# Optimization experiments

Measured on AMD Instinct MI355X. Metric: run time of the kernel, lower is better.

Reference implementation:

```python
import jax, jax.numpy as jnp
import numpy as np

B, D, C = 8192, 2048, 1000
EPS32 = float(np.finfo(np.float32).eps)      # torch clamp_probs uses finfo.eps
LOG_2PI = float(np.log(2.0 * np.pi))
GAMMA = float(1.0 / np.exp(100.0))           # lerp at global_step=0 -> start_val = 1/exp(start_rho)


def setup_inputs() -> dict:
    key = jax.random.key(0)
    k = jax.random.split(key, 6)
    feature = jax.random.normal(k[0], (B, D), jnp.float32)
    target = jax.random.randint(k[1], (B,), 0, C)
    eps = jax.random.normal(k[2], (B, D), jnp.float32)
    # y_project: Linear(C, D) -> weight [D, C], bias [D]
    y_w = jax.random.normal(k[3], (D, C), jnp.float32) * 0.02
    y_b = jnp.zeros((D,), jnp.float32)
    # cls_project: Linear(D, C) -> weight [C, D], bias [C]
    # small weights + positive bias keep Categorical probs positive (torch would
    # clamp negatives to eps; we replicate the clamp but avoid degenerate NaNs)
    cls_w = jax.random.normal(k[4], (C, D), jnp.float32) * 0.001
    cls_b = jnp.ones((C,), jnp.float32) * 5.0
    return dict(feature=feature, y_w=y_w, y_b=y_b, cls_w=cls_w, cls_b=cls_b,
                eps=eps, target=target)


def reference(feature, y_w, y_b, cls_w, cls_b, eps, target):
    # z = m.sample() : identity-covariance MVN sample, detached (torch .sample())
    z = jax.lax.stop_gradient(feature + eps)                      # [B, D]

    # y_emb = y_project(one_hot(target)) == gather of weight columns + bias
    y_emb = jnp.take(y_w, target, axis=1).T + y_b                 # [B, D]

    # Categorical(probs=cls_project(z)): normalize, clamp, log
    probs_raw = z @ cls_w.T + cls_b                               # [B, C]
    p = probs_raw / jnp.sum(probs_raw, axis=-1, keepdims=True)
    logits = jnp.log(jnp.clip(p, EPS32, 1.0 - EPS32))             # [B, C]

    # identity-covariance MVN log_prob in closed form
    const = 0.5 * D * LOG_2PI
    h1 = 0.5 * jnp.sum((z - feature) ** 2, axis=-1) + const       # -m.log_prob(z)
    h2 = 0.5 * jnp.sum((z - y_emb) ** 2, axis=-1) + const         # -y_emb_d.log_prob(z)
    h3 = -jnp.take_along_axis(logits, target[:, None], axis=1)[:, 0]

    rex = h2 - h1
    loss = jnp.mean(jnp.float32(GAMMA) * rex + h3)
    return logits, loss
```

## Files before the change

kernel.cpp:

```cpp
#include <hip/hip_runtime.h>
#include <hip/hip_bf16.h>

#define B_ROWS 8192
#define D_DIM  2048
#define C_DIM  1000
#define C_PAD  1024

#define EPS32   1.1920928955078125e-07f

typedef __attribute__((ext_vector_type(8))) short short8;
typedef __attribute__((ext_vector_type(4))) float f32x4;

#define GLOAD_LDS16(gptr, lptr) \
  __builtin_amdgcn_global_load_lds((const __attribute__((address_space(1))) void*)(gptr), \
                                   (__attribute__((address_space(3))) void*)(lptr), 16, 0, 0)

__device__ inline unsigned short f2bf(float x) {
  union { __hip_bfloat16 b; unsigned short u; } cv;
  cv.b = __float2bfloat16(x);
  return cv.u;
}

__device__ inline float wave_red(float v) {
#pragma unroll
  for (int off = 32; off > 0; off >>= 1) v += __shfl_down(v, off, 64);
  return v;
}

__global__ __launch_bounds__(256) void cast_w(const float* __restrict__ cls_w,
                                              __hip_bfloat16* __restrict__ clsw_bf) {
  int j = (blockIdx.x * 256 + threadIdx.x) * 8;
  int row = j >> 11;
  int col = j & 2047;
  union { unsigned short u[8]; uint4 v; } pk;
  if (row < C_DIM) {
    const float* src = cls_w + (size_t)row * D_DIM + col;
#pragma unroll
    for (int i2 = 0; i2 < 8; ++i2) pk.u[i2] = f2bf(src[i2]);
  } else {
#pragma unroll
    for (int i2 = 0; i2 < 8; ++i2) pk.u[i2] = 0;
  }
  *(uint4*)((unsigned short*)clsw_bf + j) = pk.v;
}

__global__ __launch_bounds__(256, 3) void gemm_fz(const float* __restrict__ feature,
                                                  const float* __restrict__ eps,
                                                  const __hip_bfloat16* __restrict__ Bt,
                                                  const float* __restrict__ cls_b,
                                                  float* __restrict__ out) {
  __shared__ __align__(16) __hip_bfloat16 sA0[64 * 64];
  __shared__ __align__(16) __hip_bfloat16 sA1[64 * 64];
  __shared__ __align__(16) __hip_bfloat16 sB0[128 * 64];
  __shared__ __align__(16) __hip_bfloat16 sB1[128 * 64];
  const int tid = threadIdx.x;
  const int m0 = blockIdx.x * 64;
  const int n0 = blockIdx.y * 128;
  const int w = tid >> 6, lane = tid & 63;
  const int wn = w * 32;
  const int l15 = lane & 15, quad = lane >> 4;

  const float* Fb[2]; const float* Eb[2]; int slotA[2];
  const __hip_bfloat16* Bb[4];           int slotB[4];
#pragma unroll
  for (int i = 0; i < 2; ++i) {
    int j = i * 256 + tid;
    int row = j >> 3;
    int cc = (j & 7) ^ (row & 7);
    Fb[i] = feature + (size_t)(m0 + row) * D_DIM + cc * 8;
    Eb[i] = eps     + (size_t)(m0 + row) * D_DIM + cc * 8;
    slotA[i] = j * 8;
  }
#pragma unroll
  for (int i = 0; i < 4; ++i) {
    int j = i * 256 + tid;
    int row = j >> 3;
    int cc = (j & 7) ^ (row & 7);
    Bb[i] = Bt + (size_t)(n0 + row) * D_DIM + cc * 8;
    slotB[i] = j * 8;
  }

  f32x4 acc[4][2] = {};
  float4 fa[2], fb[2], ea[2], eb[2];

  auto LOADA = [&](int k0) {
#pragma unroll
    for (int i = 0; i < 2; ++i) {
      fa[i] = *(const float4*)(Fb[i] + k0);
      fb[i] = *(const float4*)(Fb[i] + k0 + 4);
      ea[i] = *(const float4*)(Eb[i] + k0);
      eb[i] = *(const float4*)(Eb[i] + k0 + 4);
    }
  };
  auto GLOADB = [&](__hip_bfloat16* sB, int k0) {
#pragma unroll
    for (int i = 0; i < 4; ++i) GLOAD_LDS16(Bb[i] + k0, &sB[slotB[i]]);
  };
  auto WRITEA = [&](__hip_bfloat16* sA) {
#pragma unroll
    for (int i = 0; i < 2; ++i) {
      union { unsigned short u[8]; uint4 v; } pk;
      pk.u[0] = f2bf(fa[i].x + ea[i].x);
      pk.u[1] = f2bf(fa[i].y + ea[i].y);
      pk.u[2] = f2bf(fa[i].z + ea[i].z);
      pk.u[3] = f2bf(fa[i].w + ea[i].w);
      pk.u[4] = f2bf(fb[i].x + eb[i].x);
      pk.u[5] = f2bf(fb[i].y + eb[i].y);
      pk.u[6] = f2bf(fb[i].z + eb[i].z);
      pk.u[7] = f2bf(fb[i].w + eb[i].w);
      *(uint4*)&sA[slotA[i]] = pk.v;
    }
  };
  auto COMPUTE = [&](const __hip_bfloat16* sA, const __hip_bfloat16* sB) {
#pragma unroll
    for (int kk = 0; kk < 64; kk += 32) {
      const int ccr = (kk >> 3) + quad;
      short8 af[4], bfr[2];
#pragma unroll
      for (int i = 0; i < 4; ++i) {
        int r = i * 16 + l15;
        af[i] = *(const short8*)&sA[(r * 8 + (ccr ^ (r & 7))) * 8];
      }
#pragma unroll
      for (int jn = 0; jn < 2; ++jn) {
        int r = wn + jn * 16 + l15;
        bfr[jn] = *(const short8*)&sB[(r * 8 + (ccr ^ (r & 7))) * 8];
      }
#pragma unroll
      for (int i = 0; i < 4; ++i)
#pragma unroll
        for (int jn = 0; jn < 2; ++jn)
          acc[i][jn] = __builtin_amdgcn_mfma_f32_16x16x32_bf16(af[i], bfr[jn], acc[i][jn], 0, 0, 0);
    }
  };

  LOADA(0);
  GLOADB(sB0, 0);
  WRITEA(sA0);
  __syncthreads();

  __hip_bfloat16 *cA = sA0, *cB = sB0, *nA = sA1, *nB = sB1;
  for (int k0 = 0; k0 < D_DIM; k0 += 64) {
    const int kn = k0 + 64;
    const bool pf = kn < D_DIM;
    if (pf) {
      LOADA(kn);
      GLOADB(nB, kn);
    }
    COMPUTE(cA, cB);
    if (pf) WRITEA(nA);
    __syncthreads();
    __hip_bfloat16* t;
    t = cA; cA = nA; nA = t;
    t = cB; cB = nB; nB = t;
  }

#pragma unroll
  for (int i = 0; i < 4; ++i) {
    int row = m0 + i * 16 + quad * 4;
#pragma unroll
    for (int jn = 0; jn < 2; ++jn) {
      int col = n0 + wn + jn * 16 + l15;
      if (col < C_DIM) {
        float bias = cls_b[col];
#pragma unroll
        for (int r = 0; r < 4; ++r)
          out[(size_t)(row + r) * C_DIM + col] = acc[i][jn][r] + bias;
      }
    }
  }
}

__global__ __launch_bounds__(256) void rownorm(float* __restrict__ out,
                                               const int* __restrict__ target,
                                               float* __restrict__ rowloss) {
  int b = blockIdx.x * 4 + (threadIdx.x >> 6);
  int lane = threadIdx.x & 63;
  float* row = out + (size_t)b * C_DIM;

  float v[16];
  float s = 0.f;
#pragma unroll
  for (int k = 0; k < 4; ++k) {
    int c = k * 256 + lane * 4;
    if (c + 3 < C_DIM) {
      float4 f = *(const float4*)(row + c);
      v[k * 4 + 0] = f.x; v[k * 4 + 1] = f.y; v[k * 4 + 2] = f.z; v[k * 4 + 3] = f.w;
    } else {
#pragma unroll
      for (int i = 0; i < 4; ++i) v[k * 4 + i] = (c + i < C_DIM) ? row[c + i] : 0.f;
    }
    s += v[k * 4 + 0] + v[k * 4 + 1] + v[k * 4 + 2] + v[k * 4 + 3];
  }
  s = wave_red(s);
  float inv = 1.0f / __shfl(s, 0, 64);
  int t = target[b];

#pragma unroll
  for (int k = 0; k < 4; ++k) {
    int c = k * 256 + lane * 4;
    float lg[4];
#pragma unroll
    for (int i = 0; i < 4; ++i) {
      float p = v[k * 4 + i] * inv;
      p = fminf(fmaxf(p, EPS32), 1.0f - EPS32);
      lg[i] = __logf(p);
      if (c + i == t) rowloss[b] = -lg[i];
    }
    if (c + 3 < C_DIM) {
      *(float4*)(row + c) = make_float4(lg[0], lg[1], lg[2], lg[3]);
    } else {
#pragma unroll
      for (int i = 0; i < 4; ++i) if (c + i < C_DIM) row[c + i] = lg[i];
    }
  }
}

__global__ __launch_bounds__(256) void finalize(const float* __restrict__ rowloss,
                                                float* __restrict__ out_loss) {
  int tid = threadIdx.x;
  float s = 0.f;
  for (int i = tid; i < B_ROWS; i += 256) s += rowloss[i];
  s = wave_red(s);
  __shared__ float sm[4];
  if ((tid & 63) == 0) sm[tid >> 6] = s;
  __syncthreads();
  if (tid == 0) out_loss[0] = (sm[0] + sm[1] + sm[2] + sm[3]) * (1.0f / B_ROWS);
}

extern "C" void kernel_launch(void* const* d_in, const int* in_sizes, int n_in,
                              void* d_out, int out_size, void* d_ws, size_t ws_size,
                              hipStream_t stream) {
  const float* feature = (const float*)d_in[0];
  const float* cls_w   = (const float*)d_in[3];
  const float* cls_b   = (const float*)d_in[4];
  const float* eps     = (const float*)d_in[5];
  const int*   target  = (const int*)d_in[6];
  float* out = (float*)d_out;
  float* out_loss = out + (size_t)B_ROWS * C_DIM;

  char* ws = (char*)d_ws;
  __hip_bfloat16* clsw_bf = (__hip_bfloat16*)ws;
  float*          rowloss = (float*)(ws + 4194304);

  cast_w<<<dim3(1024), 256, 0, stream>>>(cls_w, clsw_bf);
  gemm_fz<<<dim3(B_ROWS / 64, C_PAD / 128), 256, 0, stream>>>(feature, eps, clsw_bf, cls_b, out);
  rownorm<<<dim3(B_ROWS / 4), 256, 0, stream>>>(out, target, rowloss);
  finalize<<<dim3(1), 256, 0, stream>>>(rowloss, out_loss);
}
```

Measured before the change: 266.0 us.

## Fuse GEMM, row normalization, log and loss into one full-row kernel

Replaces the tiled GEMM plus separate rownorm and finalize kernels with one kernel where each 512-thread block computes 32 full rows across all 1024 padded classes. Row sums, clamp/log and the target gather then happen in registers, avoiding a write and re-read of the 8192x1000 logits. The loss is reduced per block and accumulated with atomicAdd into a scalar that cast_w zeroes. In exchange, feature/eps are read once per row tile instead of eight times. The B operand (2 MB of bf16 weights) is now streamed fully by each of 256 blocks with a smaller K step of 32, and the block uses about 130 KB of LDS, which limits occupancy.

```diff
diff --git a/kernel.cpp b/kernel.cpp
--- a/kernel.cpp
+++ b/kernel.cpp
@@ -28,15 +28,19 @@
 }
 
 __global__ __launch_bounds__(256) void cast_w(const float* __restrict__ cls_w,
-                                              __hip_bfloat16* __restrict__ clsw_bf) {
+                                              __hip_bfloat16* __restrict__ clsw_bf,
+                                              float* __restrict__ out_loss) {
+  if (blockIdx.x == 0 && threadIdx.x == 0) out_loss[0] = 0.f;
   int j = (blockIdx.x * 256 + threadIdx.x) * 8;
   int row = j >> 11;
   int col = j & 2047;
   union { unsigned short u[8]; uint4 v; } pk;
   if (row < C_DIM) {
     const float* src = cls_w + (size_t)row * D_DIM + col;
-#pragma unroll
-    for (int i2 = 0; i2 < 8; ++i2) pk.u[i2] = f2bf(src[i2]);
+    float4 a = *(const float4*)src;
+    float4 b = *(const float4*)(src + 4);
+    pk.u[0] = f2bf(a.x); pk.u[1] = f2bf(a.y); pk.u[2] = f2bf(a.z); pk.u[3] = f2bf(a.w);
+    pk.u[4] = f2bf(b.x); pk.u[5] = f2bf(b.y); pk.u[6] = f2bf(b.z); pk.u[7] = f2bf(b.w);
   } else {
 #pragma unroll
     for (int i2 = 0; i2 < 8; ++i2) pk.u[i2] = 0;
@@ -44,94 +48,88 @@
   *(uint4*)((unsigned short*)clsw_bf + j) = pk.v;
 }
 
-__global__ __launch_bounds__(256, 3) void gemm_fz(const float* __restrict__ feature,
-                                                  const float* __restrict__ eps,
-                                                  const __hip_bfloat16* __restrict__ Bt,
-                                                  const float* __restrict__ cls_b,
-                                                  float* __restrict__ out) {
-  __shared__ __align__(16) __hip_bfloat16 sA0[64 * 64];
-  __shared__ __align__(16) __hip_bfloat16 sA1[64 * 64];
-  __shared__ __align__(16) __hip_bfloat16 sB0[128 * 64];
-  __shared__ __align__(16) __hip_bfloat16 sB1[128 * 64];
+__global__ __launch_bounds__(512, 2) void fused_all(const float* __restrict__ feature,
+                                                    const float* __restrict__ eps,
+                                                    const __hip_bfloat16* __restrict__ Bt,
+                                                    const float* __restrict__ cls_b,
+                                                    const int* __restrict__ target,
+                                                    float* __restrict__ out,
+                                                    float* __restrict__ out_loss) {
+  __shared__ __align__(16) __hip_bfloat16 sB0[C_PAD * 32];
+  __shared__ __align__(16) __hip_bfloat16 sB1[C_PAD * 32];
+  __shared__ __align__(16) __hip_bfloat16 sA0[32 * 32];
+  __shared__ __align__(16) __hip_bfloat16 sA1[32 * 32];
+  __shared__ float red[32][8];
+  __shared__ float red2[32];
+  __shared__ float wred[8];
+
   const int tid = threadIdx.x;
-  const int m0 = blockIdx.x * 64;
-  const int n0 = blockIdx.y * 128;
+  const int m0 = blockIdx.x * 32;
   const int w = tid >> 6, lane = tid & 63;
-  const int wn = w * 32;
   const int l15 = lane & 15, quad = lane >> 4;
-
-  const float* Fb[2]; const float* Eb[2]; int slotA[2];
-  const __hip_bfloat16* Bb[4];           int slotB[4];
-#pragma unroll
-  for (int i = 0; i < 2; ++i) {
-    int j = i * 256 + tid;
-    int row = j >> 3;
-    int cc = (j & 7) ^ (row & 7);
-    Fb[i] = feature + (size_t)(m0 + row) * D_DIM + cc * 8;
-    Eb[i] = eps     + (size_t)(m0 + row) * D_DIM + cc * 8;
-    slotA[i] = j * 8;
-  }
-#pragma unroll
-  for (int i = 0; i < 4; ++i) {
-    int j = i * 256 + tid;
-    int row = j >> 3;
-    int cc = (j & 7) ^ (row & 7);
-    Bb[i] = Bt + (size_t)(n0 + row) * D_DIM + cc * 8;
+  const int wn = w * 128;
+
+  const __hip_bfloat16* Bb[8]; int slotB[8];
+#pragma unroll
+  for (int i = 0; i < 8; ++i) {
+    int j = i * 512 + tid;
+    int row = j >> 2;
+    int cc = (j & 3) ^ (row & 3);
+    Bb[i] = Bt + (size_t)row * D_DIM + cc * 8;
     slotB[i] = j * 8;
   }
-
-  f32x4 acc[4][2] = {};
-  float4 fa[2], fb[2], ea[2], eb[2];
+  const float* Fp = feature; const float* Ep = eps; int slotA = 0;
+  if (tid < 128) {
+    int arow = tid >> 2;
+    int ac = (tid & 3) ^ (arow & 3);
+    Fp = feature + (size_t)(m0 + arow) * D_DIM + ac * 8;
+    Ep = eps     + (size_t)(m0 + arow) * D_DIM + ac * 8;
+    slotA = tid * 8;
+  }
+
+  f32x4 acc[2][8] = {};
+  float4 f0, f1, e0, e1;
 
   auto LOADA = [&](int k0) {
+    if (tid < 128) {
+      f0 = *(const float4*)(Fp + k0);
+      f1 = *(const float4*)(Fp + k0 + 4);
+      e0 = *(const float4*)(Ep + k0);
+      e1 = *(const float4*)(Ep + k0 + 4);
+    }
+  };
+  auto WRITEA = [&](__hip_bfloat16* sA) {
+    if (tid < 128) {
+      union { unsigned short u[8]; uint4 v; } pk;
+      pk.u[0] = f2bf(f0.x + e0.x); pk.u[1] = f2bf(f0.y + e0.y);
+      pk.u[2] = f2bf(f0.z + e0.z); pk.u[3] = f2bf(f0.w + e0.w);
+      pk.u[4] = f2bf(f1.x + e1.x); pk.u[5] = f2bf(f1.y + e1.y);
+      pk.u[6] = f2bf(f1.z + e1.z); pk.u[7] = f2bf(f1.w + e1.w);
+      *(uint4*)&sA[slotA] = pk.v;
+    }
+  };
+  auto GLOADB = [&](__hip_bfloat16* sB, int k0) {
+#pragma unroll
+    for (int i = 0; i < 8; ++i) GLOAD_LDS16(Bb[i] + k0, &sB[slotB[i]]);
+  };
+  auto COMPUTE = [&](const __hip_bfloat16* sA, const __hip_bfloat16* sB) {
+    const int ccr = quad;
+    short8 af[2], bfr[8];
 #pragma unroll
     for (int i = 0; i < 2; ++i) {
-      fa[i] = *(const float4*)(Fb[i] + k0);
-      fb[i] = *(const float4*)(Fb[i] + k0 + 4);
-      ea[i] = *(const float4*)(Eb[i] + k0);
-      eb[i] = *(const float4*)(Eb[i] + k0 + 4);
-    }
-  };
-  auto GLOADB = [&](__hip_bfloat16* sB, int k0) {
-#pragma unroll
-    for (int i = 0; i < 4; ++i) GLOAD_LDS16(Bb[i] + k0, &sB[slotB[i]]);
-  };
-  auto WRITEA = [&](__hip_bfloat16* sA) {
-#pragma unroll
-    for (int i = 0; i < 2; ++i) {
-      union { unsigned short u[8]; uint4 v; } pk;
-      pk.u[0] = f2bf(fa[i].x + ea[i].x);
-      pk.u[1] = f2bf(fa[i].y + ea[i].y);
-      pk.u[2] = f2bf(fa[i].z + ea[i].z);
-      pk.u[3] = f2bf(fa[i].w + ea[i].w);
-      pk.u[4] = f2bf(fb[i].x + eb[i].x);
-      pk.u[5] = f2bf(fb[i].y + eb[i].y);
-      pk.u[6] = f2bf(fb[i].z + eb[i].z);
-      pk.u[7] = f2bf(fb[i].w + eb[i].w);
-      *(uint4*)&sA[slotA[i]] = pk.v;
-    }
-  };
-  auto COMPUTE = [&](const __hip_bfloat16* sA, const __hip_bfloat16* sB) {
-#pragma unroll
-    for (int kk = 0; kk < 64; kk += 32) {
-      const int ccr = (kk >> 3) + quad;
-      short8 af[4], bfr[2];
-#pragma unroll
-      for (int i = 0; i < 4; ++i) {
-        int r = i * 16 + l15;
-        af[i] = *(const short8*)&sA[(r * 8 + (ccr ^ (r & 7))) * 8];
-      }
-#pragma unroll
-      for (int jn = 0; jn < 2; ++jn) {
-        int r = wn + jn * 16 + l15;
-        bfr[jn] = *(const short8*)&sB[(r * 8 + (ccr ^ (r & 7))) * 8];
-      }
-#pragma unroll
-      for (int i = 0; i < 4; ++i)
-#pragma unroll
-        for (int jn = 0; jn < 2; ++jn)
-          acc[i][jn] = __builtin_amdgcn_mfma_f32_16x16x32_bf16(af[i], bfr[jn], acc[i][jn], 0, 0, 0);
-    }
+      int r = i * 16 + l15;
+      af[i] = *(const short8*)&sA[(r * 4 + (ccr ^ (r & 3))) * 8];
+    }
+#pragma unroll
+    for (int jn = 0; jn < 8; ++jn) {
+      int r = wn + jn * 16 + l15;
+      bfr[jn] = *(const short8*)&sB[(r * 4 + (ccr ^ (r & 3))) * 8];
+    }
+#pragma unroll
+    for (int i = 0; i < 2; ++i)
+#pragma unroll
+      for (int jn = 0; jn < 8; ++jn)
+        acc[i][jn] = __builtin_amdgcn_mfma_f32_16x16x32_bf16(af[i], bfr[jn], acc[i][jn], 0, 0, 0);
   };
 
   LOADA(0);
@@ -140,9 +138,9 @@
   __syncthreads();
 
   __hip_bfloat16 *cA = sA0, *cB = sB0, *nA = sA1, *nB = sB1;
-  for (int k0 = 0; k0 < D_DIM; k0 += 64) {
-    const int kn = k0 + 64;
-    const bool pf = kn < D_DIM;
+  for (int t = 0; t < 64; ++t) {
+    const int kn = (t + 1) * 32;
+    const bool pf = t < 63;
     if (pf) {
       LOADA(kn);
       GLOADB(nB, kn);
@@ -150,82 +148,75 @@
     COMPUTE(cA, cB);
     if (pf) WRITEA(nA);
     __syncthreads();
-    __hip_bfloat16* t;
-    t = cA; cA = nA; nA = t;
-    t = cB; cB = nB; nB = t;
-  }
-
-#pragma unroll
-  for (int i = 0; i < 4; ++i) {
-    int row = m0 + i * 16 + quad * 4;
-#pragma unroll
-    for (int jn = 0; jn < 2; ++jn) {
-      int col = n0 + wn + jn * 16 + l15;
-      if (col < C_DIM) {
-        float bias = cls_b[col];
-#pragma unroll
-        for (int r = 0; r < 4; ++r)
-          out[(size_t)(row + r) * C_DIM + col] = acc[i][jn][r] + bias;
+    __hip_bfloat16* tmp;
+    tmp = cA; cA = nA; nA = tmp;
+    tmp = cB; cB = nB; nB = tmp;
+  }
+
+  float bias[8]; int bcol[8];
+#pragma unroll
+  for (int jn = 0; jn < 8; ++jn) {
+    int c = wn + jn * 16 + l15;
+    bcol[jn] = c;
+    bias[jn] = (c < C_DIM) ? cls_b[c] : 0.f;
+  }
+#pragma unroll
+  for (int i = 0; i < 2; ++i)
+#pragma unroll
+    for (int jn = 0; jn < 8; ++jn)
+#pragma unroll
+      for (int r = 0; r < 4; ++r) acc[i][jn][r] += bias[jn];
+
+#pragma unroll
+  for (int i = 0; i < 2; ++i)
+#pragma unroll
+    for (int r = 0; r < 4; ++r) {
+      float s = 0.f;
+#pragma unroll
+      for (int jn = 0; jn < 8; ++jn) s += acc[i][jn][r];
+#pragma unroll
+      for (int off = 1; off < 16; off <<= 1) s += __shfl_xor(s, off, 64);
+      if (l15 == 0) red[i * 16 + quad * 4 + r][w] = s;
+    }
+  __syncthreads();
+  if (tid < 32) {
+    float s = 0.f;
+#pragma unroll
+    for (int k = 0; k < 8; ++k) s += red[tid][k];
+    red2[tid] = 1.0f / s;
+  }
+  __syncthreads();
+
+  float lsum = 0.f;
+#pragma unroll
+  for (int i = 0; i < 2; ++i)
+#pragma unroll
+    for (int r = 0; r < 4; ++r) {
+      int R = i * 16 + quad * 4 + r;
+      float inv = red2[R];
+      int tr = target[m0 + R];
+      float* orow = out + (size_t)(m0 + R) * C_DIM;
+#pragma unroll
+      for (int jn = 0; jn < 8; ++jn) {
+        int c = bcol[jn];
+        if (c < C_DIM) {
+          float p = acc[i][jn][r] * inv;
+          p = fminf(fmaxf(p, EPS32), 1.0f - EPS32);
+          float lg = __logf(p);
+          orow[c] = lg;
+          if (c == tr) lsum -= lg;
+        }
       }
     }
-  }
-}
-
-__global__ __launch_bounds__(256) void rownorm(float* __restrict__ out,
-                                               const int* __restrict__ target,
-                                               float* __restrict__ rowloss) {
-  int b = blockIdx.x * 4 + (threadIdx.x >> 6);
-  int lane = threadIdx.x & 63;
-  float* row = out + (size_t)b * C_DIM;
-
-  float v[16];
-  float s = 0.f;
-#pragma unroll
-  for (int k = 0; k < 4; ++k) {
-    int c = k * 256 + lane * 4;
-    if (c + 3 < C_DIM) {
-      float4 f = *(const float4*)(row + c);
-      v[k * 4 + 0] = f.x; v[k * 4 + 1] = f.y; v[k * 4 + 2] = f.z; v[k * 4 + 3] = f.w;
-    } else {
-#pragma unroll
-      for (int i = 0; i < 4; ++i) v[k * 4 + i] = (c + i < C_DIM) ? row[c + i] : 0.f;
-    }
-    s += v[k * 4 + 0] + v[k * 4 + 1] + v[k * 4 + 2] + v[k * 4 + 3];
-  }
-  s = wave_red(s);
-  float inv = 1.0f / __shfl(s, 0, 64);
-  int t = target[b];
-
-#pragma unroll
-  for (int k = 0; k < 4; ++k) {
-    int c = k * 256 + lane * 4;
-    float lg[4];
-#pragma unroll
-    for (int i = 0; i < 4; ++i) {
-      float p = v[k * 4 + i] * inv;
-      p = fminf(fmaxf(p, EPS32), 1.0f - EPS32);
-      lg[i] = __logf(p);
-      if (c + i == t) rowloss[b] = -lg[i];
-    }
-    if (c + 3 < C_DIM) {
-      *(float4*)(row + c) = make_float4(lg[0], lg[1], lg[2], lg[3]);
-    } else {
-#pragma unroll
-      for (int i = 0; i < 4; ++i) if (c + i < C_DIM) row[c + i] = lg[i];
-    }
-  }
-}
-
-__global__ __launch_bounds__(256) void finalize(const float* __restrict__ rowloss,
-                                                float* __restrict__ out_loss) {
-  int tid = threadIdx.x;
-  float s = 0.f;
-  for (int i = tid; i < B_ROWS; i += 256) s += rowloss[i];
-  s = wave_red(s);
-  __shared__ float sm[4];
-  if ((tid & 63) == 0) sm[tid >> 6] = s;
-  __syncthreads();
-  if (tid == 0) out_loss[0] = (sm[0] + sm[1] + sm[2] + sm[3]) * (1.0f / B_ROWS);
+  lsum = wave_red(lsum);
+  if (lane == 0) wred[w] = lsum;
+  __syncthreads();
+  if (tid == 0) {
+    float s = 0.f;
+#pragma unroll
+    for (int k = 0; k < 8; ++k) s += wred[k];
+    atomicAdd(out_loss, s * (1.0f / B_ROWS));
+  }
 }
 
 extern "C" void kernel_launch(void* const* d_in, const int* in_sizes, int n_in,
@@ -241,10 +232,8 @@
 
   char* ws = (char*)d_ws;
   __hip_bfloat16* clsw_bf = (__hip_bfloat16*)ws;
-  float*          rowloss = (float*)(ws + 4194304);
-
-  cast_w<<<dim3(1024), 256, 0, stream>>>(cls_w, clsw_bf);
-  gemm_fz<<<dim3(B_ROWS / 64, C_PAD / 128), 256, 0, stream>>>(feature, eps, clsw_bf, cls_b, out);
-  rownorm<<<dim3(B_ROWS / 4), 256, 0, stream>>>(out, target, rowloss);
-  finalize<<<dim3(1), 256, 0, stream>>>(rowloss, out_loss);
-}
+
+  cast_w<<<dim3(1024), 256, 0, stream>>>(cls_w, clsw_bf, out_loss);
+  fused_all<<<dim3(B_ROWS / 32), 512, 0, stream>>>(feature, eps, clsw_bf, cls_b,
+                                                   target, out, out_loss);
+}
```

Measured after the change: 260.2 us. -2.2%, faster.
